# Kernel tuning notes

Measured on AMD Instinct MI355X. Metric: run time of the kernel, lower is better.

## Reference

```python
import jax, jax.numpy as jnp
import numpy as np

NEG_INF = -1e30

def masked_softmax(S, mask, axis):
    logits = jnp.where(mask > 0, S, NEG_INF)
    p = jax.nn.softmax(logits, axis=axis)
    return p * (mask > 0)


def setup_inputs() -> dict:
    key = jax.random.key(0)
    k1, k2, k3, k4 = jax.random.split(key, 4)
    B, D, Q, H = 16, 1024, 128, 1024
    U_d = jax.random.normal(k1, (B, D, H), dtype=jnp.float32)
    U_q = jax.random.normal(k2, (B, Q, H), dtype=jnp.float32)
    q_mask = jnp.ones((B, Q), dtype=jnp.int32)
    d_mask = jnp.ones((B, D), dtype=jnp.int32)
    # wc: Linear(3H -> 1), kaiming_normal on weight: std = sqrt(2 / fan_in)
    std = np.sqrt(2.0 / (3 * H))
    wc_w = jax.random.normal(k3, (3 * H,), dtype=jnp.float32) * std
    bound = 1.0 / np.sqrt(3 * H)
    wc_b = jax.random.uniform(k4, (1,), dtype=jnp.float32, minval=-bound, maxval=bound)
    return {"U_d": U_d, "U_q": U_q, "wc_w": wc_w, "wc_b": wc_b,
            "q_mask": q_mask, "d_mask": d_mask}


def reference(U_d, U_q, wc_w, wc_b, q_mask, d_mask):
    H = U_d.shape[-1]
    w_d, w_q, w_dot = wc_w[:H], wc_w[H:2 * H], wc_w[2 * H:]
    # S[b,d,q] = w_d.U_d[b,d] + w_q.U_q[b,q] + w_dot.(U_d[b,d]*U_q[b,q]) + b
    # (algebraic decomposition of Linear(cat(U_d_exp, U_q_exp, U_d_exp*U_q_exp)))
    s_d = U_d @ w_d                                  # [B, D]
    s_q = U_q @ w_q                                  # [B, Q]
    s_dot = jnp.einsum('bdh,bqh->bdq', U_d * w_dot, U_q)  # [B, D, Q]
    S = s_dot + s_d[:, :, None] + s_q[:, None, :] + wc_b[0]
    S_mask = d_mask[:, :, None] * q_mask[:, None, :]       # [B, D, Q]
    S_d2q = masked_softmax(S, S_mask, axis=-1)
    S_q2d = masked_softmax(S, S_mask, axis=-2)
    A_d2q = jnp.einsum('bdq,bqh->bdh', S_d2q, U_q)         # [B, D, H]
    A_q2d = jnp.einsum('bde,beh->bdh',
                       jnp.einsum('bdq,beq->bde', S_d2q, S_q2d), U_d)
    V_d = jnp.concatenate([U_d, A_d2q, U_d * A_d2q, U_d * A_q2d], axis=2)
    return V_d
```

## Files before the change

kernel.cpp:

```cpp
#include <hip/hip_runtime.h>
#include <hip/hip_bf16.h>


#define B_ 16
#define Dd 1024
#define Qq 128
#define Hh 1024

typedef float f32x4 __attribute__((ext_vector_type(4)));
typedef __bf16 bf16x8 __attribute__((ext_vector_type(8)));

#define MFMA(a, b, c) __builtin_amdgcn_mfma_f32_16x16x32_bf16((a), (b), (c), 0, 0, 0)

__device__ __forceinline__ bf16x8 cvt8(f32x4 a, f32x4 b) {
  bf16x8 r;
  r[0] = (__bf16)a[0]; r[1] = (__bf16)a[1]; r[2] = (__bf16)a[2]; r[3] = (__bf16)a[3];
  r[4] = (__bf16)b[0]; r[5] = (__bf16)b[1]; r[6] = (__bf16)b[2]; r[7] = (__bf16)b[3];
  return r;
}

__global__ __launch_bounds__(256) void k_cvt(const float* __restrict__ U_d,
                                             __bf16* __restrict__ Udb,
                                             __bf16* __restrict__ UdT) {
  __shared__ __bf16 lds[64][80];
  int b = blockIdx.z, d0 = blockIdx.y * 64, h0 = blockIdx.x * 64;
  int r = threadIdx.x >> 2;
  int seg = (threadIdx.x & 3) * 16;
  const float* src = U_d + ((size_t)b * Dd + d0 + r) * Hh + h0 + seg;
  __bf16* dstb = Udb + ((size_t)b * Dd + d0 + r) * Hh + h0 + seg;
  bf16x8 v[2];
#pragma unroll
  for (int g = 0; g < 2; ++g) {
    f32x4 x0 = *(const f32x4*)(src + g * 8);
    f32x4 x1 = *(const f32x4*)(src + g * 8 + 4);
    v[g] = cvt8(x0, x1);
  }
  *(bf16x8*)(dstb) = v[0];
  *(bf16x8*)(dstb + 8) = v[1];
#pragma unroll
  for (int g = 0; g < 2; ++g)
#pragma unroll
    for (int j = 0; j < 8; ++j) lds[seg + g * 8 + j][r] = v[g][j];
  __syncthreads();
  __bf16* dstt = UdT + ((size_t)b * Hh + h0 + r) * Dd + d0 + seg;
  bf16x8 w0, w1;
#pragma unroll
  for (int j = 0; j < 8; ++j) { w0[j] = lds[r][seg + j]; w1[j] = lds[r][seg + 8 + j]; }
  *(bf16x8*)dstt = w0;
  *(bf16x8*)(dstt + 8) = w1;
}

__global__ __launch_bounds__(256) void k_prep(const float* __restrict__ U_q,
                                              const float* __restrict__ wc_w,
                                              float* __restrict__ sq_part,
                                              __bf16* __restrict__ Bp,
                                              __bf16* __restrict__ U_qT) {
  __shared__ __bf16 lds_t[64][130];
  int b = blockIdx.y, h0 = blockIdx.x * 64;
  int tid = threadIdx.x;
  int q = tid >> 1, hh = (tid & 1) * 32;
  const float* urow = U_q + ((size_t)b * Qq + q) * Hh + h0 + hh;
  const float* wd = wc_w + h0 + hh;
  const float* wq = wc_w + Hh + h0 + hh;
  const float* wdot = wc_w + 2 * Hh + h0 + hh;
  __bf16* bprow = Bp + ((size_t)b * Qq + q) * Hh + h0 + hh;
  float s = 0.f;
#pragma unroll
  for (int g = 0; g < 4; ++g) {
    f32x4 u0 = *(const f32x4*)(urow + g * 8);
    f32x4 u1 = *(const f32x4*)(urow + g * 8 + 4);
    f32x4 d0 = *(const f32x4*)(wd + g * 8);
    f32x4 d1 = *(const f32x4*)(wd + g * 8 + 4);
    f32x4 q0 = *(const f32x4*)(wq + g * 8);
    f32x4 q1 = *(const f32x4*)(wq + g * 8 + 4);
    f32x4 t0 = *(const f32x4*)(wdot + g * 8);
    f32x4 t1 = *(const f32x4*)(wdot + g * 8 + 4);
    bf16x8 bp;
#pragma unroll
    for (int j = 0; j < 4; ++j) {
      bp[j] = (__bf16)(t0[j] * u0[j] + d0[j]);
      bp[4 + j] = (__bf16)(t1[j] * u1[j] + d1[j]);
      s += u0[j] * q0[j] + u1[j] * q1[j];
      lds_t[hh + g * 8 + j][q] = (__bf16)u0[j];
      lds_t[hh + g * 8 + 4 + j][q] = (__bf16)u1[j];
    }
    *(bf16x8*)(bprow + g * 8) = bp;
  }
  s += __shfl_xor(s, 1);
  if ((tid & 1) == 0) sq_part[((size_t)blockIdx.x * B_ + b) * Qq + q] = s;
  __syncthreads();
  int h = tid & 63, part = tid >> 6;
  __bf16* orow = U_qT + ((size_t)b * Hh + h0 + h) * Qq + part * 32;
#pragma unroll
  for (int g = 0; g < 4; ++g) {
    bf16x8 v;
#pragma unroll
    for (int j = 0; j < 8; ++j) v[j] = lds_t[h][part * 32 + g * 8 + j];
    *(bf16x8*)(orow + g * 8) = v;
  }
}

__global__ __launch_bounds__(256) void k_sqcomb(const float* __restrict__ sq_part,
                                                const float* __restrict__ wc_b,
                                                float* __restrict__ sq) {
  int i = blockIdx.x * 256 + threadIdx.x;
  int b = i >> 7, q = i & 127;
  float s = wc_b[0];
#pragma unroll
  for (int p = 0; p < 16; ++p) s += sq_part[((size_t)p * B_ + b) * Qq + q];
  sq[i] = s;
}

__global__ __launch_bounds__(512) void k_scores(const __bf16* __restrict__ Udb,
                                                const __bf16* __restrict__ Bp,
                                                const float* __restrict__ sq,
                                                __bf16* __restrict__ E,
                                                float* __restrict__ rmax_g,
                                                float* __restrict__ rinv_g,
                                                float* __restrict__ pm,
                                                float* __restrict__ ps) {
  __shared__ float rm_p[2][64], rs_p[2][64];
  __shared__ float cm[4][128], cs[4][128];
  int b = blockIdx.y;
  int wave = threadIdx.x >> 6, lane = threadIdx.x & 63;
  int dgrp = wave >> 1, qh = wave & 1;
  int l16 = lane & 15, quad = lane >> 4;
  int d_base = blockIdx.x * 64 + dgrp * 16;
  const __bf16* arow = Udb + ((size_t)b * Dd + d_base + l16) * Hh + quad * 8;
  const __bf16* brow = Bp + ((size_t)b * Qq + qh * 64 + l16) * Hh + quad * 8;
  f32x4 acc[4] = {};
  bf16x8 a_c = *(const bf16x8*)arow;
  bf16x8 b_c[4];
#pragma unroll
  for (int t = 0; t < 4; ++t) b_c[t] = *(const bf16x8*)(brow + (size_t)t * 16 * Hh);
  for (int k = 32; k <= Hh; k += 32) {
    int kn = (k < Hh) ? k : 0;
    bf16x8 a_n = *(const bf16x8*)(arow + kn);
    bf16x8 b_n[4];
#pragma unroll
    for (int t = 0; t < 4; ++t) b_n[t] = *(const bf16x8*)(brow + (size_t)t * 16 * Hh + kn);
#pragma unroll
    for (int t = 0; t < 4; ++t) acc[t] = MFMA(a_c, b_c[t], acc[t]);
    a_c = a_n;
#pragma unroll
    for (int t = 0; t < 4; ++t) b_c[t] = b_n[t];
  }
#pragma unroll
  for (int t = 0; t < 4; ++t) {
    float sv = sq[b * Qq + qh * 64 + t * 16 + l16];
#pragma unroll
    for (int r = 0; r < 4; ++r) acc[t][r] += sv;
  }
  int rloc_base = dgrp * 16 + quad * 4;
  float pmx[4], psm[4];
#pragma unroll
  for (int r = 0; r < 4; ++r) {
    float m = fmaxf(fmaxf(acc[0][r], acc[1][r]), fmaxf(acc[2][r], acc[3][r]));
    m = fmaxf(m, __shfl_xor(m, 1));
    m = fmaxf(m, __shfl_xor(m, 2));
    m = fmaxf(m, __shfl_xor(m, 4));
    m = fmaxf(m, __shfl_xor(m, 8));
    float s = 0.f;
#pragma unroll
    for (int t = 0; t < 4; ++t) s += __expf(acc[t][r] - m);
    s += __shfl_xor(s, 1);
    s += __shfl_xor(s, 2);
    s += __shfl_xor(s, 4);
    s += __shfl_xor(s, 8);
    pmx[r] = m;
    psm[r] = s;
  }
  if (l16 == 0) {
#pragma unroll
    for (int r = 0; r < 4; ++r) {
      rm_p[qh][rloc_base + r] = pmx[r];
      rs_p[qh][rloc_base + r] = psm[r];
    }
  }
#pragma unroll
  for (int t = 0; t < 4; ++t) {
    float m = fmaxf(fmaxf(acc[t][0], acc[t][1]), fmaxf(acc[t][2], acc[t][3]));
    m = fmaxf(m, __shfl_xor(m, 16));
    m = fmaxf(m, __shfl_xor(m, 32));
    float sc = 0.f;
#pragma unroll
    for (int r = 0; r < 4; ++r) sc += __expf(acc[t][r] - m);
    sc += __shfl_xor(sc, 16);
    sc += __shfl_xor(sc, 32);
    if (quad == 0) {
      cm[dgrp][qh * 64 + t * 16 + l16] = m;
      cs[dgrp][qh * 64 + t * 16 + l16] = sc;
    }
  }
  __syncthreads();
  float rmax[4], rinv[4];
#pragma unroll
  for (int r = 0; r < 4; ++r) {
    int rl = rloc_base + r;
    float m0 = rm_p[0][rl], m1 = rm_p[1][rl];
    float gm = fmaxf(m0, m1);
    float gs = rs_p[0][rl] * __expf(m0 - gm) + rs_p[1][rl] * __expf(m1 - gm);
    rmax[r] = gm;
    rinv[r] = 1.0f / gs;
  }
  if (qh == 0 && l16 == 0) {
#pragma unroll
    for (int r = 0; r < 4; ++r) {
      int d = d_base + quad * 4 + r;
      rmax_g[b * Dd + d] = rmax[r];
      rinv_g[b * Dd + d] = rinv[r];
    }
  }
#pragma unroll
  for (int r = 0; r < 4; ++r) {
    int d = d_base + quad * 4 + r;
#pragma unroll
    for (int t = 0; t < 4; ++t)
      E[((size_t)b * Dd + d) * Qq + qh * 64 + t * 16 + l16] =
          (__bf16)__expf(acc[t][r] - rmax[r]);
  }
  if (threadIdx.x < 128) {
    int q = threadIdx.x;
    float gm = fmaxf(fmaxf(cm[0][q], cm[1][q]), fmaxf(cm[2][q], cm[3][q]));
    float gs = 0.f;
#pragma unroll
    for (int w = 0; w < 4; ++w) gs += cs[w][q] * __expf(cm[w][q] - gm);
    size_t idx = ((size_t)b * 16 + blockIdx.x) * Qq + q;
    pm[idx] = gm;
    ps[idx] = gs;
  }
}

__global__ __launch_bounds__(256) void k_colcomb(const float* __restrict__ pm,
                                                 const float* __restrict__ ps,
                                                 float* __restrict__ cmax,
                                                 float* __restrict__ csum) {
  int i = blockIdx.x * 256 + threadIdx.x;
  int b = i >> 7, q = i & 127;
  float gm = -1e30f;
#pragma unroll
  for (int p = 0; p < 16; ++p) gm = fmaxf(gm, pm[((size_t)b * 16 + p) * Qq + q]);
  float s = 0.f;
#pragma unroll
  for (int p = 0; p < 16; ++p)
    s += ps[((size_t)b * 16 + p) * Qq + q] * __expf(pm[((size_t)b * 16 + p) * Qq + q] - gm);
  cmax[i] = gm;
  csum[i] = s;
}

__global__ __launch_bounds__(256) void k_q2dT(const __bf16* __restrict__ E,
                                              const float* __restrict__ rmax_g,
                                              const float* __restrict__ cmax,
                                              const float* __restrict__ csum,
                                              __bf16* __restrict__ Sq2dT) {
  __shared__ float tile[32][33];
  int b = blockIdx.z;
  int d0 = blockIdx.y * 32, q0 = blockIdx.x * 32;
  int tx = threadIdx.x & 31, ty = threadIdx.x >> 5;
#pragma unroll
  for (int i = 0; i < 4; ++i) {
    int rr = ty + i * 8;
    tile[rr][tx] = (float)E[((size_t)b * Dd + d0 + rr) * Qq + q0 + tx];
  }
  float rm = rmax_g[b * Dd + d0 + tx];
  __syncthreads();
#pragma unroll
  for (int i = 0; i < 4; ++i) {
    int rr = ty + i * 8;
    int q = q0 + rr;
    float scale = __expf(rm - cmax[b * Qq + q]) / csum[b * Qq + q];
    Sq2dT[((size_t)b * Qq + q) * Dd + d0 + tx] = (__bf16)(tile[tx][rr] * scale);
  }
}

__global__ __launch_bounds__(512) void k_mt(const __bf16* __restrict__ UdT,
                                            const __bf16* __restrict__ Sq2dT,
                                            __bf16* __restrict__ MT) {
  int b = blockIdx.y;
  int wave = threadIdx.x >> 6, lane = threadIdx.x & 63;
  int hgrp = wave >> 1, qh = wave & 1;
  int l16 = lane & 15, quad = lane >> 4;
  int h_base = blockIdx.x * 64 + hgrp * 16;
  const __bf16* arow = UdT + ((size_t)b * Hh + h_base + l16) * Dd + quad * 8;
  const __bf16* brow = Sq2dT + ((size_t)b * Qq + qh * 64 + l16) * Dd + quad * 8;
  f32x4 acc[4] = {};
  bf16x8 a_c = *(const bf16x8*)arow;
  bf16x8 b_c[4];
#pragma unroll
  for (int t = 0; t < 4; ++t) b_c[t] = *(const bf16x8*)(brow + (size_t)t * 16 * Dd);
  for (int k = 32; k <= Dd; k += 32) {
    int kn = (k < Dd) ? k : 0;
    bf16x8 a_n = *(const bf16x8*)(arow + kn);
    bf16x8 b_n[4];
#pragma unroll
    for (int t = 0; t < 4; ++t) b_n[t] = *(const bf16x8*)(brow + (size_t)t * 16 * Dd + kn);
#pragma unroll
    for (int t = 0; t < 4; ++t) acc[t] = MFMA(a_c, b_c[t], acc[t]);
    a_c = a_n;
#pragma unroll
    for (int t = 0; t < 4; ++t) b_c[t] = b_n[t];
  }
#pragma unroll
  for (int r = 0; r < 4; ++r) {
    int h = h_base + quad * 4 + r;
#pragma unroll
    for (int t = 0; t < 4; ++t)
      MT[((size_t)b * Hh + h) * Qq + qh * 64 + t * 16 + l16] = (__bf16)acc[t][r];
  }
}

__global__ __launch_bounds__(256) void k_out(const __bf16* __restrict__ E,
                                             const float* __restrict__ rinv_g,
                                             const __bf16* __restrict__ U_qT,
                                             const __bf16* __restrict__ MT,
                                             const float* __restrict__ U_d,
                                             float* __restrict__ out) {
  int b = blockIdx.z;
  int wave = threadIdx.x >> 6, lane = threadIdx.x & 63;
  int l16 = lane & 15, quad = lane >> 4;
  int d_base = blockIdx.x * 64 + wave * 16;
  int h_base = blockIdx.y * 128;
  const __bf16* arow = E + ((size_t)b * Dd + d_base + l16) * Qq + quad * 8;
  const __bf16* BU = U_qT + ((size_t)b * Hh + h_base + l16) * Qq + quad * 8;
  const __bf16* BM = MT + ((size_t)b * Hh + h_base + l16) * Qq + quad * 8;
  f32x4 aU[8] = {}, aM[8] = {};
#pragma unroll
  for (int k = 0; k < Qq; k += 32) {
    bf16x8 a = *(const bf16x8*)(arow + k);
#pragma unroll
    for (int t = 0; t < 8; ++t) {
      bf16x8 b1 = *(const bf16x8*)(BU + (size_t)t * 16 * Qq + k);
      aU[t] = MFMA(a, b1, aU[t]);
      bf16x8 b2 = *(const bf16x8*)(BM + (size_t)t * 16 * Qq + k);
      aM[t] = MFMA(a, b2, aM[t]);
    }
  }
#pragma unroll
  for (int r = 0; r < 4; ++r) {
    int d = d_base + quad * 4 + r;
    float rv = rinv_g[b * Dd + d];
    const float* ur = U_d + ((size_t)b * Dd + d) * Hh;
    float* o = out + ((size_t)b * Dd + d) * (4 * Hh);
#pragma unroll
    for (int t = 0; t < 8; ++t) {
      int h = h_base + t * 16 + l16;
      float u = ur[h];
      float a1 = aU[t][r] * rv;
      float a2 = aM[t][r] * rv;
      o[h] = u;
      o[Hh + h] = a1;
      o[2 * Hh + h] = u * a1;
      o[3 * Hh + h] = u * a2;
    }
  }
}

extern "C" void kernel_launch(void* const* d_in, const int* in_sizes, int n_in,
                              void* d_out, int out_size, void* d_ws, size_t ws_size,
                              hipStream_t stream) {
  const float* U_d = (const float*)d_in[0];
  const float* U_q = (const float*)d_in[1];
  const float* wc_w = (const float*)d_in[2];
  const float* wc_b = (const float*)d_in[3];
  float* out = (float*)d_out;

  char* ws = (char*)d_ws;
  size_t off = 0;
  auto alloc = [&](size_t bytes) {
    size_t o = off;
    off += (bytes + 255) & ~(size_t)255;
    return o;
  };
  float* sq_part = (float*)(ws + alloc((size_t)16 * B_ * Qq * 4));
  float* sq = (float*)(ws + alloc((size_t)B_ * Qq * 4));
  float* rmax_g = (float*)(ws + alloc((size_t)B_ * Dd * 4));
  float* rinv_g = (float*)(ws + alloc((size_t)B_ * Dd * 4));
  float* pm = (float*)(ws + alloc((size_t)B_ * 16 * Qq * 4));
  float* ps = (float*)(ws + alloc((size_t)B_ * 16 * Qq * 4));
  float* cmax = (float*)(ws + alloc((size_t)B_ * Qq * 4));
  float* csum = (float*)(ws + alloc((size_t)B_ * Qq * 4));
  __bf16* E = (__bf16*)(ws + alloc((size_t)B_ * Dd * Qq * 2));
  __bf16* Sq2dT = (__bf16*)(ws + alloc((size_t)B_ * Dd * Qq * 2));
  __bf16* Bp = (__bf16*)(ws + alloc((size_t)B_ * Qq * Hh * 2));
  __bf16* U_qT = (__bf16*)(ws + alloc((size_t)B_ * Qq * Hh * 2));
  __bf16* MT = (__bf16*)(ws + alloc((size_t)B_ * Hh * Qq * 2));
  __bf16* Udb = (__bf16*)(ws + alloc((size_t)B_ * Dd * Hh * 2));
  __bf16* UdT = (__bf16*)(ws + alloc((size_t)B_ * Hh * Dd * 2));

  k_cvt<<<dim3(Hh / 64, Dd / 64, B_), 256, 0, stream>>>(U_d, Udb, UdT);
  k_prep<<<dim3(Hh / 64, B_), 256, 0, stream>>>(U_q, wc_w, sq_part, Bp, U_qT);
  k_sqcomb<<<dim3(B_ * Qq / 256), 256, 0, stream>>>(sq_part, wc_b, sq);
  k_scores<<<dim3(Dd / 64, B_), 512, 0, stream>>>(Udb, Bp, sq, E, rmax_g, rinv_g, pm, ps);
  k_colcomb<<<dim3(B_ * Qq / 256), 256, 0, stream>>>(pm, ps, cmax, csum);
  k_q2dT<<<dim3(Qq / 32, Dd / 32, B_), 256, 0, stream>>>(E, rmax_g, cmax, csum, Sq2dT);
  k_mt<<<dim3(Hh / 64, B_), 512, 0, stream>>>(UdT, Sq2dT, MT);
  k_out<<<dim3(Dd / 64, Hh / 128, B_), 256, 0, stream>>>(E, rinv_g, U_qT, MT, U_d, out);
}
```

Measured before the change: 500.6 us.

## Fuse combine kernels into consumers and vectorize output stores in k_out

Removes the k_sqcomb and k_colcomb launches by computing the q-score sum inside k_scores (via shared memory) and the column max/sum inside each k_q2dT block. Rewrites k_out with swapped MFMA operand roles so each lane owns four consecutive h values, enabling 16-byte vector loads of U_d and stores to the output, with a smaller h tile per block. This reduces launch overhead and store transaction count, at the cost of redundant column-stat recomputation across the d-blocks of k_q2dT.

```diff
diff --git a/kernel.cpp b/kernel.cpp
--- a/kernel.cpp
+++ b/kernel.cpp
@@ -100,28 +100,26 @@
   }
 }
 
-__global__ __launch_bounds__(256) void k_sqcomb(const float* __restrict__ sq_part,
-                                                const float* __restrict__ wc_b,
-                                                float* __restrict__ sq) {
-  int i = blockIdx.x * 256 + threadIdx.x;
-  int b = i >> 7, q = i & 127;
-  float s = wc_b[0];
-#pragma unroll
-  for (int p = 0; p < 16; ++p) s += sq_part[((size_t)p * B_ + b) * Qq + q];
-  sq[i] = s;
-}
-
 __global__ __launch_bounds__(512) void k_scores(const __bf16* __restrict__ Udb,
                                                 const __bf16* __restrict__ Bp,
-                                                const float* __restrict__ sq,
+                                                const float* __restrict__ sq_part,
+                                                const float* __restrict__ wc_b,
                                                 __bf16* __restrict__ E,
                                                 float* __restrict__ rmax_g,
                                                 float* __restrict__ rinv_g,
                                                 float* __restrict__ pm,
                                                 float* __restrict__ ps) {
+  __shared__ float sq_s[128];
   __shared__ float rm_p[2][64], rs_p[2][64];
   __shared__ float cm[4][128], cs[4][128];
   int b = blockIdx.y;
+  if (threadIdx.x < 128) {
+    int q = threadIdx.x;
+    float s = wc_b[0];
+#pragma unroll
+    for (int p = 0; p < 16; ++p) s += sq_part[((size_t)p * B_ + b) * Qq + q];
+    sq_s[q] = s;
+  }
   int wave = threadIdx.x >> 6, lane = threadIdx.x & 63;
   int dgrp = wave >> 1, qh = wave & 1;
   int l16 = lane & 15, quad = lane >> 4;
@@ -145,9 +143,10 @@
 #pragma unroll
     for (int t = 0; t < 4; ++t) b_c[t] = b_n[t];
   }
+  __syncthreads();
 #pragma unroll
   for (int t = 0; t < 4; ++t) {
-    float sv = sq[b * Qq + qh * 64 + t * 16 + l16];
+    float sv = sq_s[qh * 64 + t * 16 + l16];
 #pragma unroll
     for (int r = 0; r < 4; ++r) acc[t][r] += sv;
   }
@@ -231,29 +230,13 @@
   }
 }
 
-__global__ __launch_bounds__(256) void k_colcomb(const float* __restrict__ pm,
-                                                 const float* __restrict__ ps,
-                                                 float* __restrict__ cmax,
-                                                 float* __restrict__ csum) {
-  int i = blockIdx.x * 256 + threadIdx.x;
-  int b = i >> 7, q = i & 127;
-  float gm = -1e30f;
-#pragma unroll
-  for (int p = 0; p < 16; ++p) gm = fmaxf(gm, pm[((size_t)b * 16 + p) * Qq + q]);
-  float s = 0.f;
-#pragma unroll
-  for (int p = 0; p < 16; ++p)
-    s += ps[((size_t)b * 16 + p) * Qq + q] * __expf(pm[((size_t)b * 16 + p) * Qq + q] - gm);
-  cmax[i] = gm;
-  csum[i] = s;
-}
-
 __global__ __launch_bounds__(256) void k_q2dT(const __bf16* __restrict__ E,
                                               const float* __restrict__ rmax_g,
-                                              const float* __restrict__ cmax,
-                                              const float* __restrict__ csum,
+                                              const float* __restrict__ pm,
+                                              const float* __restrict__ ps,
                                               __bf16* __restrict__ Sq2dT) {
   __shared__ float tile[32][33];
+  __shared__ float cmx_s[32], cinv_s[32];
   int b = blockIdx.z;
   int d0 = blockIdx.y * 32, q0 = blockIdx.x * 32;
   int tx = threadIdx.x & 31, ty = threadIdx.x >> 5;
@@ -263,13 +246,24 @@
     tile[rr][tx] = (float)E[((size_t)b * Dd + d0 + rr) * Qq + q0 + tx];
   }
   float rm = rmax_g[b * Dd + d0 + tx];
+  if (threadIdx.x < 32) {
+    int q = q0 + threadIdx.x;
+    float gm = -1e30f;
+#pragma unroll
+    for (int p = 0; p < 16; ++p) gm = fmaxf(gm, pm[((size_t)b * 16 + p) * Qq + q]);
+    float s = 0.f;
+#pragma unroll
+    for (int p = 0; p < 16; ++p)
+      s += ps[((size_t)b * 16 + p) * Qq + q] * __expf(pm[((size_t)b * 16 + p) * Qq + q] - gm);
+    cmx_s[threadIdx.x] = gm;
+    cinv_s[threadIdx.x] = 1.0f / s;
+  }
   __syncthreads();
 #pragma unroll
   for (int i = 0; i < 4; ++i) {
     int rr = ty + i * 8;
-    int q = q0 + rr;
-    float scale = __expf(rm - cmax[b * Qq + q]) / csum[b * Qq + q];
-    Sq2dT[((size_t)b * Qq + q) * Dd + d0 + tx] = (__bf16)(tile[tx][rr] * scale);
+    float scale = __expf(rm - cmx_s[rr]) * cinv_s[rr];
+    Sq2dT[((size_t)b * Qq + q0 + rr) * Dd + d0 + tx] = (__bf16)(tile[tx][rr] * scale);
   }
 }
 
@@ -318,40 +312,43 @@
   int b = blockIdx.z;
   int wave = threadIdx.x >> 6, lane = threadIdx.x & 63;
   int l16 = lane & 15, quad = lane >> 4;
-  int d_base = blockIdx.x * 64 + wave * 16;
-  int h_base = blockIdx.y * 128;
-  const __bf16* arow = E + ((size_t)b * Dd + d_base + l16) * Qq + quad * 8;
-  const __bf16* BU = U_qT + ((size_t)b * Hh + h_base + l16) * Qq + quad * 8;
-  const __bf16* BM = MT + ((size_t)b * Hh + h_base + l16) * Qq + quad * 8;
-  f32x4 aU[8] = {}, aM[8] = {};
+  int d0 = blockIdx.x * 64;
+  int hb = blockIdx.y * 64 + wave * 16;
+  const __bf16* aUrow = U_qT + ((size_t)b * Hh + hb + l16) * Qq + quad * 8;
+  const __bf16* aMrow = MT + ((size_t)b * Hh + hb + l16) * Qq + quad * 8;
+  const __bf16* brow = E + ((size_t)b * Dd + d0 + l16) * Qq + quad * 8;
+  f32x4 aU[4] = {}, aM[4] = {};
 #pragma unroll
   for (int k = 0; k < Qq; k += 32) {
-    bf16x8 a = *(const bf16x8*)(arow + k);
-#pragma unroll
-    for (int t = 0; t < 8; ++t) {
-      bf16x8 b1 = *(const bf16x8*)(BU + (size_t)t * 16 * Qq + k);
-      aU[t] = MFMA(a, b1, aU[t]);
-      bf16x8 b2 = *(const bf16x8*)(BM + (size_t)t * 16 * Qq + k);
-      aM[t] = MFMA(a, b2, aM[t]);
-    }
-  }
-#pragma unroll
-  for (int r = 0; r < 4; ++r) {
-    int d = d_base + quad * 4 + r;
+    bf16x8 au = *(const bf16x8*)(aUrow + k);
+    bf16x8 am = *(const bf16x8*)(aMrow + k);
+#pragma unroll
+    for (int t = 0; t < 4; ++t) {
+      bf16x8 be = *(const bf16x8*)(brow + (size_t)t * 16 * Qq + k);
+      aU[t] = MFMA(au, be, aU[t]);
+      aM[t] = MFMA(am, be, aM[t]);
+    }
+  }
+  int h4 = hb + quad * 4;
+#pragma unroll
+  for (int t = 0; t < 4; ++t) {
+    int d = d0 + t * 16 + l16;
     float rv = rinv_g[b * Dd + d];
-    const float* ur = U_d + ((size_t)b * Dd + d) * Hh;
+    const float* ur = U_d + ((size_t)b * Dd + d) * Hh + h4;
     float* o = out + ((size_t)b * Dd + d) * (4 * Hh);
-#pragma unroll
-    for (int t = 0; t < 8; ++t) {
-      int h = h_base + t * 16 + l16;
-      float u = ur[h];
-      float a1 = aU[t][r] * rv;
-      float a2 = aM[t][r] * rv;
-      o[h] = u;
-      o[Hh + h] = a1;
-      o[2 * Hh + h] = u * a1;
-      o[3 * Hh + h] = u * a2;
-    }
+    f32x4 u = *(const f32x4*)ur;
+    f32x4 a1, a2, p1, p2;
+#pragma unroll
+    for (int j = 0; j < 4; ++j) {
+      a1[j] = aU[t][j] * rv;
+      a2[j] = aM[t][j] * rv;
+      p1[j] = u[j] * a1[j];
+      p2[j] = u[j] * a2[j];
+    }
+    *(f32x4*)(o + h4) = u;
+    *(f32x4*)(o + Hh + h4) = a1;
+    *(f32x4*)(o + 2 * Hh + h4) = p1;
+    *(f32x4*)(o + 3 * Hh + h4) = p2;
   }
 }
 
@@ -372,13 +369,10 @@
     return o;
   };
   float* sq_part = (float*)(ws + alloc((size_t)16 * B_ * Qq * 4));
-  float* sq = (float*)(ws + alloc((size_t)B_ * Qq * 4));
   float* rmax_g = (float*)(ws + alloc((size_t)B_ * Dd * 4));
   float* rinv_g = (float*)(ws + alloc((size_t)B_ * Dd * 4));
   float* pm = (float*)(ws + alloc((size_t)B_ * 16 * Qq * 4));
   float* ps = (float*)(ws + alloc((size_t)B_ * 16 * Qq * 4));
-  float* cmax = (float*)(ws + alloc((size_t)B_ * Qq * 4));
-  float* csum = (float*)(ws + alloc((size_t)B_ * Qq * 4));
   __bf16* E = (__bf16*)(ws + alloc((size_t)B_ * Dd * Qq * 2));
   __bf16* Sq2dT = (__bf16*)(ws + alloc((size_t)B_ * Dd * Qq * 2));
   __bf16* Bp = (__bf16*)(ws + alloc((size_t)B_ * Qq * Hh * 2));
@@ -389,10 +383,8 @@
 
   k_cvt<<<dim3(Hh / 64, Dd / 64, B_), 256, 0, stream>>>(U_d, Udb, UdT);
   k_prep<<<dim3(Hh / 64, B_), 256, 0, stream>>>(U_q, wc_w, sq_part, Bp, U_qT);
-  k_sqcomb<<<dim3(B_ * Qq / 256), 256, 0, stream>>>(sq_part, wc_b, sq);
-  k_scores<<<dim3(Dd / 64, B_), 512, 0, stream>>>(Udb, Bp, sq, E, rmax_g, rinv_g, pm, ps);
-  k_colcomb<<<dim3(B_ * Qq / 256), 256, 0, stream>>>(pm, ps, cmax, csum);
-  k_q2dT<<<dim3(Qq / 32, Dd / 32, B_), 256, 0, stream>>>(E, rmax_g, cmax, csum, Sq2dT);
+  k_scores<<<dim3(Dd / 64, B_), 512, 0, stream>>>(Udb, Bp, sq_part, wc_b, E, rmax_g, rinv_g, pm, ps);
+  k_q2dT<<<dim3(Qq / 32, Dd / 32, B_), 256, 0, stream>>>(E, rmax_g, pm, ps, Sq2dT);
   k_mt<<<dim3(Hh / 64, B_), 512, 0, stream>>>(UdT, Sq2dT, MT);
-  k_out<<<dim3(Dd / 64, Hh / 128, B_), 256, 0, stream>>>(E, rinv_g, U_qT, MT, U_d, out);
-}
+  k_out<<<dim3(Dd / 64, Hh / 64, B_), 256, 0, stream>>>(E, rinv_g, U_qT, MT, U_d, out);
+}
```

Result: faster. 477.6 us (-4.6%).
